# Kernel optimization log

Measured on AMD Instinct MI355X. Metric: run time of the kernel, lower is better.

The kernel has to match this reference:

```python
import jax, jax.numpy as jnp
import numpy as np

N_HEAD = 16
HEAD_DIM = 128  # module's n_embd (per-head)
SEQ = 2048
BATCH = 4
D_MODEL = N_HEAD * HEAD_DIM  # 2048, also input feature dim


def setup_inputs() -> dict:
    key = jax.random.key(0)
    ks = jax.random.split(key, 7)
    scale = 1.0 / np.sqrt(D_MODEL)
    x = jax.random.normal(ks[0], (BATCH, SEQ, D_MODEL), dtype=jnp.float32)
    Wq = jax.random.normal(ks[1], (D_MODEL, D_MODEL), dtype=jnp.float32) * scale
    Wk = jax.random.normal(ks[2], (D_MODEL, D_MODEL), dtype=jnp.float32) * scale
    Wv = jax.random.normal(ks[3], (D_MODEL, D_MODEL), dtype=jnp.float32) * scale
    bq = jnp.zeros((D_MODEL,), dtype=jnp.float32)
    bk = jnp.zeros((D_MODEL,), dtype=jnp.float32)
    bv = jnp.zeros((D_MODEL,), dtype=jnp.float32)
    return {"x": x, "Wq": Wq, "bq": bq, "Wk": Wk, "bk": bk, "Wv": Wv, "bv": bv}


def reference(x, Wq, bq, Wk, bk, Wv, bv):
    B, S, _ = x.shape
    H, D = N_HEAD, HEAD_DIM
    # QKV projections, split heads: [B, H, S, D]
    q = (x @ Wq + bq).reshape(B, S, H, D).transpose(0, 2, 1, 3)
    k = (x @ Wk + bk).reshape(B, S, H, D).transpose(0, 2, 1, 3)
    v = (x @ Wv + bv).reshape(B, S, H, D).transpose(0, 2, 1, 3)
    # scaled dot-product scores [B, H, S, S]
    att = jnp.einsum('bhqd,bhkd->bhqk', q, k) * (1.0 / jnp.sqrt(jnp.float32(D)))
    # causal mask: query i attends to keys j <= i
    causal = jnp.tril(jnp.ones((S, S), dtype=bool))
    att = jnp.where(causal, att, -jnp.inf)
    att = jax.nn.softmax(att, axis=-1)
    # dropout is deterministic (train=False) -> identity
    y = jnp.einsum('bhqk,bhkd->bhqd', att, v)  # [B, H, S, D]
    return y.transpose(0, 2, 1, 3).reshape(B, S, H * D)
```

## Files before the change

### kernel.cpp

```cpp
#include <hip/hip_runtime.h>
#include <hip/hip_bf16.h>
#include <stdint.h>

#define DEVI __device__ __forceinline__

using bf16 = __hip_bfloat16;

typedef __bf16 bf16x8 __attribute__((ext_vector_type(8)));
typedef float f32x4 __attribute__((ext_vector_type(4)));

constexpr int BATCH = 4, NH = 16, SEQ = 2048, HD = 128, DMODEL = 2048;
constexpr int MROWS = BATCH * SEQ;

DEVI f32x4 mfma16(uint4 a, uint4 b, f32x4 c) {
  return __builtin_amdgcn_mfma_f32_16x16x32_bf16(
      __builtin_bit_cast(bf16x8, a), __builtin_bit_cast(bf16x8, b), c, 0, 0, 0);
}

DEVI unsigned pack2(float a, float b) {
  __hip_bfloat16 ha = __float2bfloat16(a), hb = __float2bfloat16(b);
  unsigned short ua = __builtin_bit_cast(unsigned short, ha);
  unsigned short ub = __builtin_bit_cast(unsigned short, hb);
  return ((unsigned)ub << 16) | (unsigned)ua;
}

DEVI void gload16(const void* g, void* l) {
  auto gp = reinterpret_cast<__attribute__((address_space(1))) unsigned int*>(
      reinterpret_cast<uintptr_t>(g));
  auto lp = reinterpret_cast<__attribute__((address_space(3))) unsigned int*>(
      reinterpret_cast<uintptr_t>(l));
  __builtin_amdgcn_global_load_lds(gp, lp, 16, 0, 0);
}

__global__ void cast_x_kernel(const float* __restrict__ in, bf16* __restrict__ out, int n8) {
  for (int i = blockIdx.x * blockDim.x + threadIdx.x; i < n8; i += gridDim.x * blockDim.x) {
    const float4* p = (const float4*)in + (size_t)i * 2;
    float4 a = p[0], b = p[1];
    uint4 u;
    u.x = pack2(a.x, a.y);
    u.y = pack2(a.z, a.w);
    u.z = pack2(b.x, b.y);
    u.w = pack2(b.z, b.w);
    *((uint4*)out + i) = u;
  }
}

__global__ void transpose_w_kernel(const float* __restrict__ W0, const float* __restrict__ W1,
                                   const float* __restrict__ W2, bf16* __restrict__ WtBase) {
  const int z = blockIdx.z;
  const float* W = (z == 0) ? W0 : (z == 1) ? W1 : W2;
  bf16* Wt = WtBase + (size_t)z * DMODEL * DMODEL;
  __shared__ float tile[64][65];
  const int k0 = blockIdx.x * 64, n0 = blockIdx.y * 64;
  const int tid = threadIdx.x;
  for (int i = tid; i < 4096; i += 256) {
    int r = i >> 6, c = i & 63;
    tile[r][c] = W[(size_t)(k0 + r) * DMODEL + n0 + c];
  }
  __syncthreads();
  for (int i = tid; i < 4096; i += 256) {
    int r = i >> 6, c = i & 63;
    Wt[(size_t)(n0 + r) * DMODEL + k0 + c] = __float2bfloat16(tile[c][r]);
  }
}

__global__ __launch_bounds__(256) void gemm_bf16(
    const bf16* __restrict__ A, const bf16* __restrict__ Bt,
    const float* __restrict__ bias, bf16* __restrict__ Cout, int transposed) {
  __shared__ __align__(16) bf16 As[128][32];
  __shared__ __align__(16) bf16 Bs[128][32];
  const int tid = threadIdx.x;
  const int lane = tid & 63, wave = tid >> 6;
  const int lr = lane & 15, lg = lane >> 4;
  const int m0 = blockIdx.x * 128, n0 = blockIdx.y * 128;
  const int wr = wave >> 1, wc = wave & 1;

  f32x4 acc[4][4];
#pragma unroll
  for (int i = 0; i < 4; ++i)
#pragma unroll
    for (int j = 0; j < 4; ++j) acc[i][j] = (f32x4){0.f, 0.f, 0.f, 0.f};

  const char* ag = (const char*)(A + (size_t)(m0 + (tid >> 2)) * DMODEL) + (tid & 3) * 16;
  const char* bg = (const char*)(Bt + (size_t)(n0 + (tid >> 2)) * DMODEL) + (tid & 3) * 16;
  char* asw = (char*)As + wave * 1024;
  char* bsw = (char*)Bs + wave * 1024;
  constexpr size_t rowadv = (size_t)64 * DMODEL * 2;

  for (int k0 = 0; k0 < DMODEL; k0 += 32) {
    gload16(ag + k0 * 2, asw);
    gload16(ag + k0 * 2 + rowadv, asw + 4096);
    gload16(bg + k0 * 2, bsw);
    gload16(bg + k0 * 2 + rowadv, bsw + 4096);
    __syncthreads();
    uint4 af[4], bfr[4];
#pragma unroll
    for (int i = 0; i < 4; ++i) af[i] = *(const uint4*)&As[wr * 64 + i * 16 + lr][lg * 8];
#pragma unroll
    for (int j = 0; j < 4; ++j) bfr[j] = *(const uint4*)&Bs[wc * 64 + j * 16 + lr][lg * 8];
#pragma unroll
    for (int i = 0; i < 4; ++i)
#pragma unroll
      for (int j = 0; j < 4; ++j) acc[i][j] = mfma16(af[i], bfr[j], acc[i][j]);
    __syncthreads();
  }

  float bvals[4];
#pragma unroll
  for (int nf = 0; nf < 4; ++nf) bvals[nf] = bias[n0 + wc * 64 + nf * 16 + lr];

  const int bh = ((m0 >> 11) << 4) | (n0 >> 7);
  const int sbase = (m0 & 2047) + wr * 64;
  if (!transposed) {
    bf16* base = Cout + (size_t)bh * SEQ * HD;
#pragma unroll
    for (int mf = 0; mf < 4; ++mf)
#pragma unroll
      for (int nf = 0; nf < 4; ++nf) {
        int d = wc * 64 + nf * 16 + lr;
#pragma unroll
        for (int jj = 0; jj < 4; ++jj) {
          int s = sbase + mf * 16 + lg * 4 + jj;
          base[(size_t)s * HD + d] = __float2bfloat16(acc[mf][nf][jj] + bvals[nf]);
        }
      }
  } else {
    bf16* base = Cout + (size_t)bh * HD * SEQ;
#pragma unroll
    for (int mf = 0; mf < 4; ++mf)
#pragma unroll
      for (int nf = 0; nf < 4; ++nf) {
        int d = wc * 64 + nf * 16 + lr;
        int s0 = sbase + mf * 16 + lg * 4;
        uint2 u;
        u.x = pack2(acc[mf][nf][0] + bvals[nf], acc[mf][nf][1] + bvals[nf]);
        u.y = pack2(acc[mf][nf][2] + bvals[nf], acc[mf][nf][3] + bvals[nf]);
        *(uint2*)&base[(size_t)d * SEQ + s0] = u;
      }
  }
}

__global__ __launch_bounds__(256) void attn_kernel(
    const bf16* __restrict__ Q, const bf16* __restrict__ K,
    const bf16* __restrict__ Vt, float* __restrict__ out) {
  extern __shared__ __align__(16) char smem[];
  char* KsB = smem;
  char* VsB = smem + 32768;
  char* plB = smem + 65536;

  const int tid = threadIdx.x;
  const int lane = tid & 63;
  const int wave = tid >> 6;
  const int lr = lane & 15, lg = lane >> 4;
  const unsigned swl = ((unsigned)(lr & 7)) << 4;

  const int lid = blockIdx.x;
  const int xcd = lid & 7, slot = lid >> 3;
  const int bh = xcd * 8 + (slot >> 3);
  const int pi = slot & 7;
  const int b = bh >> 4, h = bh & 15;

  const bf16* Qp = Q + (size_t)bh * SEQ * HD;
  const char* Kg0 = (const char*)(K + (size_t)bh * SEQ * HD);
  const char* Vg0 = (const char*)(Vt + (size_t)bh * HD * SEQ);
  char* pbase = plB + wave * 4096;

  const float C2 = 0.08838834764831845f * 1.44269504088896f;
  int cur = 0;

  for (int sec = 0; sec < 2; ++sec) {
    const int qt = (sec == 0) ? pi : (15 - pi);
    const int q0 = qt * 128 + wave * 32;
    const int nt = 2 * qt + 2;
    const int nt_w = (q0 + 95) >> 6;

    uint4 qfrag[2][4];
#pragma unroll
    for (int qf = 0; qf < 2; ++qf) {
      const bf16* qrow = Qp + (size_t)(q0 + qf * 16 + lr) * HD + lg * 8;
#pragma unroll
      for (int dc = 0; dc < 4; ++dc) qfrag[qf][dc] = *(const uint4*)(qrow + dc * 32);
    }

    f32x4 acc[8][2];
#pragma unroll
    for (int df = 0; df < 8; ++df) {
      acc[df][0] = (f32x4){0.f, 0.f, 0.f, 0.f};
      acc[df][1] = (f32x4){0.f, 0.f, 0.f, 0.f};
    }
    float m_run[2] = {-1e30f, -1e30f};
    float l_run[2] = {0.f, 0.f};
    const int qg[2] = {q0 + lr, q0 + 16 + lr};

    {
      const char* Kg = Kg0;
      const char* Vg = Vg0;
      char* kl = KsB + cur * 16384 + wave * 1024;
      char* vl = VsB + cur * 16384 + wave * 1024;
#pragma unroll
      for (int r = 0; r < 4; ++r) {
        int o = r * 4096 + tid * 16;
        int krow = o >> 8; unsigned kcb = o & 255;
        gload16(Kg + krow * 256 + (kcb ^ (((unsigned)(krow & 7)) << 4)), kl + r * 4096);
        int vrow = o >> 7; unsigned vcb = o & 127;
        gload16(Vg + (size_t)vrow * 4096 + (vcb ^ (((unsigned)(vrow & 7)) << 4)), vl + r * 4096);
      }
    }
    __syncthreads();

    for (int t = 0; t < nt; ++t) {
      if (t + 1 < nt) {
        const char* Kg = Kg0 + ((size_t)(t + 1) << 14);
        const char* Vg = Vg0 + ((size_t)(t + 1) << 7);
        char* kl = KsB + (cur ^ 1) * 16384 + wave * 1024;
        char* vl = VsB + (cur ^ 1) * 16384 + wave * 1024;
#pragma unroll
        for (int r = 0; r < 4; ++r) {
          int o = r * 4096 + tid * 16;
          int krow = o >> 8; unsigned kcb = o & 255;
          gload16(Kg + krow * 256 + (kcb ^ (((unsigned)(krow & 7)) << 4)), kl + r * 4096);
          int vrow = o >> 7; unsigned vcb = o & 127;
          gload16(Vg + (size_t)vrow * 4096 + (vcb ^ (((unsigned)(vrow & 7)) << 4)), vl + r * 4096);
        }
      }

      if (t < nt_w) {
        const int kv0 = t << 6;
        const char* kb = KsB + cur * 16384;
        const char* vb = VsB + cur * 16384;

        f32x4 sfr[4][2];
#pragma unroll
        for (int kvf = 0; kvf < 4; ++kvf) {
          sfr[kvf][0] = (f32x4){0.f, 0.f, 0.f, 0.f};
          sfr[kvf][1] = (f32x4){0.f, 0.f, 0.f, 0.f};
          const char* krow = kb + (kvf * 16 + lr) * 256;
#pragma unroll
          for (int dc = 0; dc < 4; ++dc) {
            uint4 ka = *(const uint4*)(krow + (((unsigned)(dc * 64 + lg * 16)) ^ swl));
            sfr[kvf][0] = mfma16(ka, qfrag[0][dc], sfr[kvf][0]);
            sfr[kvf][1] = mfma16(ka, qfrag[1][dc], sfr[kvf][1]);
          }
        }

        const bool need_mask = (kv0 + 63) > q0;
#pragma unroll
        for (int qf = 0; qf < 2; ++qf) {
          float mx = -1e30f;
#pragma unroll
          for (int kvf = 0; kvf < 4; ++kvf)
#pragma unroll
            for (int j = 0; j < 4; ++j) {
              float v = sfr[kvf][qf][j] * C2;
              if (need_mask) {
                int kvgl = kv0 + kvf * 16 + lg * 4 + j;
                v = (kvgl <= qg[qf]) ? v : -1e30f;
              }
              sfr[kvf][qf][j] = v;
              mx = fmaxf(mx, v);
            }
          mx = fmaxf(mx, __shfl_xor(mx, 16));
          mx = fmaxf(mx, __shfl_xor(mx, 32));
          float mnew = fmaxf(m_run[qf], mx);
          float corr = exp2f(m_run[qf] - mnew);
          m_run[qf] = mnew;
          float ps = 0.f;
          const int qlocal = qf * 16 + lr;
          const unsigned sw = ((unsigned)(qlocal & 7)) << 4;
          char* bp = pbase + qlocal * 128;
#pragma unroll
          for (int kvf = 0; kvf < 4; ++kvf) {
            float p0 = exp2f(sfr[kvf][qf][0] - mnew);
            float p1 = exp2f(sfr[kvf][qf][1] - mnew);
            float p2 = exp2f(sfr[kvf][qf][2] - mnew);
            float p3 = exp2f(sfr[kvf][qf][3] - mnew);
            ps += p0 + p1 + p2 + p3;
            unsigned off = ((unsigned)(kvf * 32 + lg * 8)) ^ sw;
            *(unsigned*)(bp + off) = pack2(p0, p1);
            *(unsigned*)(bp + off + 4) = pack2(p2, p3);
          }
          ps += __shfl_xor(ps, 16);
          ps += __shfl_xor(ps, 32);
          l_run[qf] = l_run[qf] * corr + ps;
#pragma unroll
          for (int df = 0; df < 8; ++df) acc[df][qf] *= corr;
        }
        asm volatile("s_waitcnt lgkmcnt(0)" ::: "memory");

        uint4 pb[2][2];
#pragma unroll
        for (int qf = 0; qf < 2; ++qf) {
          const int qlocal = qf * 16 + lr;
          const unsigned sw = ((unsigned)(qlocal & 7)) << 4;
          char* bp = pbase + qlocal * 128;
          pb[0][qf] = *(uint4*)(bp + (((unsigned)(lg * 16)) ^ sw));
          pb[1][qf] = *(uint4*)(bp + (((unsigned)(64 + lg * 16)) ^ sw));
        }

#pragma unroll
        for (int df = 0; df < 8; ++df) {
          const char* vrow = vb + (df * 16 + lr) * 128;
          uint4 va0 = *(const uint4*)(vrow + (((unsigned)(lg * 16)) ^ swl));
          uint4 va1 = *(const uint4*)(vrow + (((unsigned)(64 + lg * 16)) ^ swl));
          acc[df][0] = mfma16(va0, pb[0][0], acc[df][0]);
          acc[df][1] = mfma16(va0, pb[0][1], acc[df][1]);
          acc[df][0] = mfma16(va1, pb[1][0], acc[df][0]);
          acc[df][1] = mfma16(va1, pb[1][1], acc[df][1]);
        }
      }

      __syncthreads();
      cur ^= 1;
    }

#pragma unroll
    for (int qf = 0; qf < 2; ++qf) {
      float inv = 1.f / l_run[qf];
      size_t rowoff = ((size_t)b * SEQ + (size_t)(q0 + qf * 16 + lr)) * DMODEL + h * HD;
#pragma unroll
      for (int df = 0; df < 8; ++df) {
        float4 o;
        o.x = acc[df][qf][0] * inv;
        o.y = acc[df][qf][1] * inv;
        o.z = acc[df][qf][2] * inv;
        o.w = acc[df][qf][3] * inv;
        *(float4*)(out + rowoff + df * 16 + lg * 4) = o;
      }
    }
  }
}

extern "C" void kernel_launch(void* const* d_in, const int* in_sizes, int n_in,
                              void* d_out, int out_size, void* d_ws, size_t ws_size,
                              hipStream_t stream) {
  const float* x = (const float*)d_in[0];
  const float* Wq = (const float*)d_in[1];
  const float* bq = (const float*)d_in[2];
  const float* Wk = (const float*)d_in[3];
  const float* bk = (const float*)d_in[4];
  const float* Wv = (const float*)d_in[5];
  const float* bv = (const float*)d_in[6];
  float* out = (float*)d_out;

  const size_t sz_x = (size_t)MROWS * DMODEL * 2;
  const size_t sz_w = (size_t)DMODEL * DMODEL * 2;
  const size_t sz_qkv = (size_t)MROWS * DMODEL * 2;
  if (ws_size < sz_x + 3 * sz_w + 3 * sz_qkv) return;

  char* w = (char*)d_ws;
  bf16* xb = (bf16*)w;  w += sz_x;
  bf16* WtQ = (bf16*)w; w += sz_w;
  bf16* WtK = (bf16*)w; w += sz_w;
  bf16* WtV = (bf16*)w; w += sz_w;
  bf16* Qb = (bf16*)w;  w += sz_qkv;
  bf16* Kb = (bf16*)w;  w += sz_qkv;
  bf16* Vtb = (bf16*)w; w += sz_qkv;

  cast_x_kernel<<<2048, 256, 0, stream>>>(x, xb, MROWS * DMODEL / 8);
  transpose_w_kernel<<<dim3(32, 32, 3), 256, 0, stream>>>(Wq, Wk, Wv, WtQ);
  gemm_bf16<<<dim3(64, 16), 256, 0, stream>>>(xb, WtQ, bq, Qb, 0);
  gemm_bf16<<<dim3(64, 16), 256, 0, stream>>>(xb, WtK, bk, Kb, 0);
  gemm_bf16<<<dim3(64, 16), 256, 0, stream>>>(xb, WtV, bv, Vtb, 1);
  attn_kernel<<<dim3(512), 256, 81920, stream>>>(Qb, Kb, Vtb, out);
}
```

Before: 636.5 us.

## Double-buffer GEMM tiles and restructure attention with 512 threads, direct V loads

The projection GEMM gets double-buffered shared-memory tiles so the next K-slice loads while MFMAs run on the current one, and one barrier per iteration is dropped. The attention kernel moves to 8 waves of 16 query rows each, stops staging V in LDS and reads V fragments straight from global memory, and shrinks LDS use so more blocks can fit per CU. It also adds a lazy softmax rescale that skips correcting the accumulator unless the row max grows past a threshold. The direct V reads rely on cache hits instead of LDS reuse, and the lazy rescale risks larger intermediate exponent values.

```diff
diff --git a/kernel.cpp b/kernel.cpp
--- a/kernel.cpp
+++ b/kernel.cpp
@@ -67,8 +67,8 @@
 __global__ __launch_bounds__(256) void gemm_bf16(
     const bf16* __restrict__ A, const bf16* __restrict__ Bt,
     const float* __restrict__ bias, bf16* __restrict__ Cout, int transposed) {
-  __shared__ __align__(16) bf16 As[128][32];
-  __shared__ __align__(16) bf16 Bs[128][32];
+  __shared__ __align__(16) bf16 As[2][128][32];
+  __shared__ __align__(16) bf16 Bs[2][128][32];
   const int tid = threadIdx.x;
   const int lane = tid & 63, wave = tid >> 6;
   const int lr = lane & 15, lg = lane >> 4;
@@ -87,22 +87,32 @@
   char* bsw = (char*)Bs + wave * 1024;
   constexpr size_t rowadv = (size_t)64 * DMODEL * 2;
 
+  gload16(ag, asw);
+  gload16(ag + rowadv, asw + 4096);
+  gload16(bg, bsw);
+  gload16(bg + rowadv, bsw + 4096);
+  __syncthreads();
+
+  int cur = 0;
   for (int k0 = 0; k0 < DMODEL; k0 += 32) {
-    gload16(ag + k0 * 2, asw);
-    gload16(ag + k0 * 2 + rowadv, asw + 4096);
-    gload16(bg + k0 * 2, bsw);
-    gload16(bg + k0 * 2 + rowadv, bsw + 4096);
-    __syncthreads();
+    if (k0 + 32 < DMODEL) {
+      int nb = (cur ^ 1) * 8192;
+      gload16(ag + (k0 + 32) * 2, asw + nb);
+      gload16(ag + (k0 + 32) * 2 + rowadv, asw + nb + 4096);
+      gload16(bg + (k0 + 32) * 2, bsw + nb);
+      gload16(bg + (k0 + 32) * 2 + rowadv, bsw + nb + 4096);
+    }
     uint4 af[4], bfr[4];
 #pragma unroll
-    for (int i = 0; i < 4; ++i) af[i] = *(const uint4*)&As[wr * 64 + i * 16 + lr][lg * 8];
-#pragma unroll
-    for (int j = 0; j < 4; ++j) bfr[j] = *(const uint4*)&Bs[wc * 64 + j * 16 + lr][lg * 8];
+    for (int i = 0; i < 4; ++i) af[i] = *(const uint4*)&As[cur][wr * 64 + i * 16 + lr][lg * 8];
+#pragma unroll
+    for (int j = 0; j < 4; ++j) bfr[j] = *(const uint4*)&Bs[cur][wc * 64 + j * 16 + lr][lg * 8];
 #pragma unroll
     for (int i = 0; i < 4; ++i)
 #pragma unroll
       for (int j = 0; j < 4; ++j) acc[i][j] = mfma16(af[i], bfr[j], acc[i][j]);
     __syncthreads();
+    cur ^= 1;
   }
 
   float bvals[4];
@@ -140,13 +150,12 @@
   }
 }
 
-__global__ __launch_bounds__(256) void attn_kernel(
+__global__ __launch_bounds__(512, 4) void attn_kernel(
     const bf16* __restrict__ Q, const bf16* __restrict__ K,
     const bf16* __restrict__ Vt, float* __restrict__ out) {
   extern __shared__ __align__(16) char smem[];
   char* KsB = smem;
-  char* VsB = smem + 32768;
-  char* plB = smem + 65536;
+  char* plB = smem + 32768;
 
   const int tid = threadIdx.x;
   const int lane = tid & 63;
@@ -162,48 +171,39 @@
 
   const bf16* Qp = Q + (size_t)bh * SEQ * HD;
   const char* Kg0 = (const char*)(K + (size_t)bh * SEQ * HD);
-  const char* Vg0 = (const char*)(Vt + (size_t)bh * HD * SEQ);
-  char* pbase = plB + wave * 4096;
+  const bf16* Vp = Vt + (size_t)bh * HD * SEQ;
+  char* bp = plB + wave * 2304 + lr * 144;
 
   const float C2 = 0.08838834764831845f * 1.44269504088896f;
+  const float THR = 8.0f;
   int cur = 0;
 
   for (int sec = 0; sec < 2; ++sec) {
     const int qt = (sec == 0) ? pi : (15 - pi);
-    const int q0 = qt * 128 + wave * 32;
+    const int q0 = qt * 128 + wave * 16;
     const int nt = 2 * qt + 2;
-    const int nt_w = (q0 + 95) >> 6;
-
-    uint4 qfrag[2][4];
-#pragma unroll
-    for (int qf = 0; qf < 2; ++qf) {
-      const bf16* qrow = Qp + (size_t)(q0 + qf * 16 + lr) * HD + lg * 8;
-#pragma unroll
-      for (int dc = 0; dc < 4; ++dc) qfrag[qf][dc] = *(const uint4*)(qrow + dc * 32);
-    }
-
-    f32x4 acc[8][2];
-#pragma unroll
-    for (int df = 0; df < 8; ++df) {
-      acc[df][0] = (f32x4){0.f, 0.f, 0.f, 0.f};
-      acc[df][1] = (f32x4){0.f, 0.f, 0.f, 0.f};
-    }
-    float m_run[2] = {-1e30f, -1e30f};
-    float l_run[2] = {0.f, 0.f};
-    const int qg[2] = {q0 + lr, q0 + 16 + lr};
-
+    const int nt_w = (q0 + 79) >> 6;
+    const int qg = q0 + lr;
+
+    uint4 qfrag[4];
     {
-      const char* Kg = Kg0;
-      const char* Vg = Vg0;
-      char* kl = KsB + cur * 16384 + wave * 1024;
-      char* vl = VsB + cur * 16384 + wave * 1024;
-#pragma unroll
-      for (int r = 0; r < 4; ++r) {
-        int o = r * 4096 + tid * 16;
+      const bf16* qrow = Qp + (size_t)qg * HD + lg * 8;
+#pragma unroll
+      for (int dc = 0; dc < 4; ++dc) qfrag[dc] = *(const uint4*)(qrow + dc * 32);
+    }
+
+    f32x4 acc[8];
+#pragma unroll
+    for (int df = 0; df < 8; ++df) acc[df] = (f32x4){0.f, 0.f, 0.f, 0.f};
+    float m_run = -1e30f, l_run = 0.f;
+
+    {
+      char* kl = KsB + cur * 16384 + tid * 16;
+#pragma unroll
+      for (int r = 0; r < 2; ++r) {
+        int o = r * 8192 + tid * 16;
         int krow = o >> 8; unsigned kcb = o & 255;
-        gload16(Kg + krow * 256 + (kcb ^ (((unsigned)(krow & 7)) << 4)), kl + r * 4096);
-        int vrow = o >> 7; unsigned vcb = o & 127;
-        gload16(Vg + (size_t)vrow * 4096 + (vcb ^ (((unsigned)(vrow & 7)) << 4)), vl + r * 4096);
+        gload16(Kg0 + krow * 256 + (kcb ^ (((unsigned)(krow & 7)) << 4)), kl + r * 8192);
       }
     }
     __syncthreads();
@@ -211,101 +211,83 @@
     for (int t = 0; t < nt; ++t) {
       if (t + 1 < nt) {
         const char* Kg = Kg0 + ((size_t)(t + 1) << 14);
-        const char* Vg = Vg0 + ((size_t)(t + 1) << 7);
-        char* kl = KsB + (cur ^ 1) * 16384 + wave * 1024;
-        char* vl = VsB + (cur ^ 1) * 16384 + wave * 1024;
-#pragma unroll
-        for (int r = 0; r < 4; ++r) {
-          int o = r * 4096 + tid * 16;
+        char* kl = KsB + (cur ^ 1) * 16384 + tid * 16;
+#pragma unroll
+        for (int r = 0; r < 2; ++r) {
+          int o = r * 8192 + tid * 16;
           int krow = o >> 8; unsigned kcb = o & 255;
-          gload16(Kg + krow * 256 + (kcb ^ (((unsigned)(krow & 7)) << 4)), kl + r * 4096);
-          int vrow = o >> 7; unsigned vcb = o & 127;
-          gload16(Vg + (size_t)vrow * 4096 + (vcb ^ (((unsigned)(vrow & 7)) << 4)), vl + r * 4096);
+          gload16(Kg + krow * 256 + (kcb ^ (((unsigned)(krow & 7)) << 4)), kl + r * 8192);
         }
       }
 
       if (t < nt_w) {
         const int kv0 = t << 6;
         const char* kb = KsB + cur * 16384;
-        const char* vb = VsB + cur * 16384;
-
-        f32x4 sfr[4][2];
+
+        f32x4 sfr[4];
 #pragma unroll
         for (int kvf = 0; kvf < 4; ++kvf) {
-          sfr[kvf][0] = (f32x4){0.f, 0.f, 0.f, 0.f};
-          sfr[kvf][1] = (f32x4){0.f, 0.f, 0.f, 0.f};
+          sfr[kvf] = (f32x4){0.f, 0.f, 0.f, 0.f};
           const char* krow = kb + (kvf * 16 + lr) * 256;
 #pragma unroll
           for (int dc = 0; dc < 4; ++dc) {
             uint4 ka = *(const uint4*)(krow + (((unsigned)(dc * 64 + lg * 16)) ^ swl));
-            sfr[kvf][0] = mfma16(ka, qfrag[0][dc], sfr[kvf][0]);
-            sfr[kvf][1] = mfma16(ka, qfrag[1][dc], sfr[kvf][1]);
+            sfr[kvf] = mfma16(ka, qfrag[dc], sfr[kvf]);
           }
         }
 
         const bool need_mask = (kv0 + 63) > q0;
-#pragma unroll
-        for (int qf = 0; qf < 2; ++qf) {
-          float mx = -1e30f;
-#pragma unroll
-          for (int kvf = 0; kvf < 4; ++kvf)
-#pragma unroll
-            for (int j = 0; j < 4; ++j) {
-              float v = sfr[kvf][qf][j] * C2;
-              if (need_mask) {
-                int kvgl = kv0 + kvf * 16 + lg * 4 + j;
-                v = (kvgl <= qg[qf]) ? v : -1e30f;
-              }
-              sfr[kvf][qf][j] = v;
-              mx = fmaxf(mx, v);
+        float mx = -1e30f;
+#pragma unroll
+        for (int kvf = 0; kvf < 4; ++kvf)
+#pragma unroll
+          for (int j = 0; j < 4; ++j) {
+            float v = sfr[kvf][j] * C2;
+            if (need_mask) {
+              int kvgl = kv0 + kvf * 16 + lg * 4 + j;
+              v = (kvgl <= qg) ? v : -1e30f;
             }
-          mx = fmaxf(mx, __shfl_xor(mx, 16));
-          mx = fmaxf(mx, __shfl_xor(mx, 32));
-          float mnew = fmaxf(m_run[qf], mx);
-          float corr = exp2f(m_run[qf] - mnew);
-          m_run[qf] = mnew;
-          float ps = 0.f;
-          const int qlocal = qf * 16 + lr;
-          const unsigned sw = ((unsigned)(qlocal & 7)) << 4;
-          char* bp = pbase + qlocal * 128;
-#pragma unroll
-          for (int kvf = 0; kvf < 4; ++kvf) {
-            float p0 = exp2f(sfr[kvf][qf][0] - mnew);
-            float p1 = exp2f(sfr[kvf][qf][1] - mnew);
-            float p2 = exp2f(sfr[kvf][qf][2] - mnew);
-            float p3 = exp2f(sfr[kvf][qf][3] - mnew);
-            ps += p0 + p1 + p2 + p3;
-            unsigned off = ((unsigned)(kvf * 32 + lg * 8)) ^ sw;
-            *(unsigned*)(bp + off) = pack2(p0, p1);
-            *(unsigned*)(bp + off + 4) = pack2(p2, p3);
+            sfr[kvf][j] = v;
+            mx = fmaxf(mx, v);
           }
-          ps += __shfl_xor(ps, 16);
-          ps += __shfl_xor(ps, 32);
-          l_run[qf] = l_run[qf] * corr + ps;
-#pragma unroll
-          for (int df = 0; df < 8; ++df) acc[df][qf] *= corr;
-        }
+        mx = fmaxf(mx, __shfl_xor(mx, 16));
+        mx = fmaxf(mx, __shfl_xor(mx, 32));
+        if (!__all(mx <= m_run + THR)) {
+          float mnew = fmaxf(m_run, mx);
+          float corr = exp2f(m_run - mnew);
+          l_run *= corr;
+#pragma unroll
+          for (int df = 0; df < 8; ++df) acc[df] *= corr;
+          m_run = mnew;
+        }
+        float ps = 0.f;
+#pragma unroll
+        for (int kvf = 0; kvf < 4; ++kvf) {
+          float p0 = exp2f(sfr[kvf][0] - m_run);
+          float p1 = exp2f(sfr[kvf][1] - m_run);
+          float p2 = exp2f(sfr[kvf][2] - m_run);
+          float p3 = exp2f(sfr[kvf][3] - m_run);
+          ps += p0 + p1 + p2 + p3;
+          unsigned off = (unsigned)(kvf * 32 + lg * 8);
+          *(unsigned*)(bp + off) = pack2(p0, p1);
+          *(unsigned*)(bp + off + 4) = pack2(p2, p3);
+        }
+        ps += __shfl_xor(ps, 16);
+        ps += __shfl_xor(ps, 32);
+        l_run += ps;
+
         asm volatile("s_waitcnt lgkmcnt(0)" ::: "memory");
 
-        uint4 pb[2][2];
-#pragma unroll
-        for (int qf = 0; qf < 2; ++qf) {
-          const int qlocal = qf * 16 + lr;
-          const unsigned sw = ((unsigned)(qlocal & 7)) << 4;
-          char* bp = pbase + qlocal * 128;
-          pb[0][qf] = *(uint4*)(bp + (((unsigned)(lg * 16)) ^ sw));
-          pb[1][qf] = *(uint4*)(bp + (((unsigned)(64 + lg * 16)) ^ sw));
-        }
+        uint4 pb0 = *(uint4*)(bp + lg * 16);
+        uint4 pb1 = *(uint4*)(bp + 64 + lg * 16);
 
 #pragma unroll
         for (int df = 0; df < 8; ++df) {
-          const char* vrow = vb + (df * 16 + lr) * 128;
-          uint4 va0 = *(const uint4*)(vrow + (((unsigned)(lg * 16)) ^ swl));
-          uint4 va1 = *(const uint4*)(vrow + (((unsigned)(64 + lg * 16)) ^ swl));
-          acc[df][0] = mfma16(va0, pb[0][0], acc[df][0]);
-          acc[df][1] = mfma16(va0, pb[0][1], acc[df][1]);
-          acc[df][0] = mfma16(va1, pb[1][0], acc[df][0]);
-          acc[df][1] = mfma16(va1, pb[1][1], acc[df][1]);
+          const bf16* vrow = Vp + (size_t)(df * 16 + lr) * SEQ + kv0 + lg * 8;
+          uint4 va0 = *(const uint4*)(vrow);
+          uint4 va1 = *(const uint4*)(vrow + 32);
+          acc[df] = mfma16(va0, pb0, acc[df]);
+          acc[df] = mfma16(va1, pb1, acc[df]);
         }
       }
 
@@ -313,17 +295,16 @@
       cur ^= 1;
     }
 
-#pragma unroll
-    for (int qf = 0; qf < 2; ++qf) {
-      float inv = 1.f / l_run[qf];
-      size_t rowoff = ((size_t)b * SEQ + (size_t)(q0 + qf * 16 + lr)) * DMODEL + h * HD;
+    {
+      float inv = 1.f / l_run;
+      size_t rowoff = ((size_t)b * SEQ + (size_t)qg) * DMODEL + h * HD;
 #pragma unroll
       for (int df = 0; df < 8; ++df) {
         float4 o;
-        o.x = acc[df][qf][0] * inv;
-        o.y = acc[df][qf][1] * inv;
-        o.z = acc[df][qf][2] * inv;
-        o.w = acc[df][qf][3] * inv;
+        o.x = acc[df][0] * inv;
+        o.y = acc[df][1] * inv;
+        o.z = acc[df][2] * inv;
+        o.w = acc[df][3] * inv;
         *(float4*)(out + rowoff + df * 16 + lg * 4) = o;
       }
     }
@@ -361,5 +342,5 @@
   gemm_bf16<<<dim3(64, 16), 256, 0, stream>>>(xb, WtQ, bq, Qb, 0);
   gemm_bf16<<<dim3(64, 16), 256, 0, stream>>>(xb, WtK, bk, Kb, 0);
   gemm_bf16<<<dim3(64, 16), 256, 0, stream>>>(xb, WtV, bv, Vtb, 1);
-  attn_kernel<<<dim3(512), 256, 81920, stream>>>(Qb, Kb, Vtb, out);
-}
+  attn_kernel<<<dim3(512), 512, 51200, stream>>>(Qb, Kb, Vtb, out);
+}
```

New measurement: 708.2 us. 1.11x slower.

## Double-buffer GEMM, keep P in registers, lazy softmax rescale in attention

Applied to the files above, without the earlier changes.

The GEMM gets double-buffered LDS tiles so the next K-slice loads overlap the MFMAs, an XCD-aware block remap, and a swapped operand order for Q/K so the epilogue writes packed, vectorized rows. Attention drops the LDS round trip for P by feeding register fragments straight into 16x16x16 bf16 MFMAs, and rescales the running max only when it grows past a threshold. It also shrinks shared memory and sets launch bounds to allow two blocks per CU. The trade-offs are twice as many PV MFMA instructions, higher register pressure, and the numeric assumption that exp2 stays bounded when the max is not updated.

```diff
diff --git a/kernel.cpp b/kernel.cpp
--- a/kernel.cpp
+++ b/kernel.cpp
@@ -7,14 +7,27 @@
 using bf16 = __hip_bfloat16;
 
 typedef __bf16 bf16x8 __attribute__((ext_vector_type(8)));
+typedef short s16x4 __attribute__((ext_vector_type(4)));
 typedef float f32x4 __attribute__((ext_vector_type(4)));
 
 constexpr int BATCH = 4, NH = 16, SEQ = 2048, HD = 128, DMODEL = 2048;
 constexpr int MROWS = BATCH * SEQ;
 
-DEVI f32x4 mfma16(uint4 a, uint4 b, f32x4 c) {
+DEVI f32x4 mfma32(uint4 a, uint4 b, f32x4 c) {
   return __builtin_amdgcn_mfma_f32_16x16x32_bf16(
       __builtin_bit_cast(bf16x8, a), __builtin_bit_cast(bf16x8, b), c, 0, 0, 0);
+}
+
+DEVI f32x4 mfma16k(uint2 a, uint2 b, f32x4 c) {
+#if __has_builtin(__builtin_amdgcn_mfma_f32_16x16x16bf16_1k)
+  return __builtin_amdgcn_mfma_f32_16x16x16bf16_1k(
+      __builtin_bit_cast(s16x4, a), __builtin_bit_cast(s16x4, b), c, 0, 0, 0);
+#else
+  f32x4 d;
+  asm("v_mfma_f32_16x16x16_bf16 %0, %1, %2, %3"
+      : "=v"(d) : "v"(a), "v"(b), "v"(c));
+  return d;
+#endif
 }
 
 DEVI unsigned pack2(float a, float b) {
@@ -64,15 +77,19 @@
   }
 }
 
+template <int TR>
 __global__ __launch_bounds__(256) void gemm_bf16(
     const bf16* __restrict__ A, const bf16* __restrict__ Bt,
-    const float* __restrict__ bias, bf16* __restrict__ Cout, int transposed) {
-  __shared__ __align__(16) bf16 As[128][32];
-  __shared__ __align__(16) bf16 Bs[128][32];
+    const float* __restrict__ bias, bf16* __restrict__ Cout) {
+  __shared__ __align__(16) bf16 As[2][128][32];
+  __shared__ __align__(16) bf16 Bs[2][128][32];
   const int tid = threadIdx.x;
   const int lane = tid & 63, wave = tid >> 6;
   const int lr = lane & 15, lg = lane >> 4;
-  const int m0 = blockIdx.x * 128, n0 = blockIdx.y * 128;
+  const int lid = blockIdx.y * gridDim.x + blockIdx.x;
+  const int g = lid & 7, kk = lid >> 3;
+  const int m0 = (kk & 63) * 128;
+  const int n0 = ((g << 1) | (kk >> 6)) * 128;
   const int wr = wave >> 1, wc = wave & 1;
 
   f32x4 acc[4][4];
@@ -87,44 +104,60 @@
   char* bsw = (char*)Bs + wave * 1024;
   constexpr size_t rowadv = (size_t)64 * DMODEL * 2;
 
+  gload16(ag, asw);
+  gload16(ag + rowadv, asw + 4096);
+  gload16(bg, bsw);
+  gload16(bg + rowadv, bsw + 4096);
+  __syncthreads();
+
+  int cur = 0;
   for (int k0 = 0; k0 < DMODEL; k0 += 32) {
-    gload16(ag + k0 * 2, asw);
-    gload16(ag + k0 * 2 + rowadv, asw + 4096);
-    gload16(bg + k0 * 2, bsw);
-    gload16(bg + k0 * 2 + rowadv, bsw + 4096);
+    if (k0 + 32 < DMODEL) {
+      int nb = (cur ^ 1) * 8192;
+      gload16(ag + (k0 + 32) * 2, asw + nb);
+      gload16(ag + (k0 + 32) * 2 + rowadv, asw + nb + 4096);
+      gload16(bg + (k0 + 32) * 2, bsw + nb);
+      gload16(bg + (k0 + 32) * 2 + rowadv, bsw + nb + 4096);
+    }
+    uint4 af[4], bfr[4];
+#pragma unroll
+    for (int i = 0; i < 4; ++i) af[i] = *(const uint4*)&As[cur][wr * 64 + i * 16 + lr][lg * 8];
+#pragma unroll
+    for (int j = 0; j < 4; ++j) bfr[j] = *(const uint4*)&Bs[cur][wc * 64 + j * 16 + lr][lg * 8];
+#pragma unroll
+    for (int i = 0; i < 4; ++i)
+#pragma unroll
+      for (int j = 0; j < 4; ++j) {
+        if (TR == 0)
+          acc[i][j] = mfma32(bfr[j], af[i], acc[i][j]);
+        else
+          acc[i][j] = mfma32(af[i], bfr[j], acc[i][j]);
+      }
     __syncthreads();
-    uint4 af[4], bfr[4];
-#pragma unroll
-    for (int i = 0; i < 4; ++i) af[i] = *(const uint4*)&As[wr * 64 + i * 16 + lr][lg * 8];
-#pragma unroll
-    for (int j = 0; j < 4; ++j) bfr[j] = *(const uint4*)&Bs[wc * 64 + j * 16 + lr][lg * 8];
-#pragma unroll
-    for (int i = 0; i < 4; ++i)
-#pragma unroll
-      for (int j = 0; j < 4; ++j) acc[i][j] = mfma16(af[i], bfr[j], acc[i][j]);
-    __syncthreads();
-  }
-
-  float bvals[4];
-#pragma unroll
-  for (int nf = 0; nf < 4; ++nf) bvals[nf] = bias[n0 + wc * 64 + nf * 16 + lr];
+    cur ^= 1;
+  }
 
   const int bh = ((m0 >> 11) << 4) | (n0 >> 7);
   const int sbase = (m0 & 2047) + wr * 64;
-  if (!transposed) {
+  if (TR == 0) {
     bf16* base = Cout + (size_t)bh * SEQ * HD;
 #pragma unroll
-    for (int mf = 0; mf < 4; ++mf)
-#pragma unroll
-      for (int nf = 0; nf < 4; ++nf) {
-        int d = wc * 64 + nf * 16 + lr;
-#pragma unroll
-        for (int jj = 0; jj < 4; ++jj) {
-          int s = sbase + mf * 16 + lg * 4 + jj;
-          base[(size_t)s * HD + d] = __float2bfloat16(acc[mf][nf][jj] + bvals[nf]);
-        }
-      }
+    for (int j = 0; j < 4; ++j) {
+      const int d0 = wc * 64 + j * 16 + lg * 4;
+      float4 bb = *(const float4*)&bias[n0 + d0];
+#pragma unroll
+      for (int i = 0; i < 4; ++i) {
+        int s = sbase + i * 16 + lr;
+        uint2 u;
+        u.x = pack2(acc[i][j][0] + bb.x, acc[i][j][1] + bb.y);
+        u.y = pack2(acc[i][j][2] + bb.z, acc[i][j][3] + bb.w);
+        *(uint2*)&base[(size_t)s * HD + d0] = u;
+      }
+    }
   } else {
+    float bvals[4];
+#pragma unroll
+    for (int nf = 0; nf < 4; ++nf) bvals[nf] = bias[n0 + wc * 64 + nf * 16 + lr];
     bf16* base = Cout + (size_t)bh * HD * SEQ;
 #pragma unroll
     for (int mf = 0; mf < 4; ++mf)
@@ -140,13 +173,12 @@
   }
 }
 
-__global__ __launch_bounds__(256) void attn_kernel(
+__global__ __launch_bounds__(256, 2) void attn_kernel(
     const bf16* __restrict__ Q, const bf16* __restrict__ K,
     const bf16* __restrict__ Vt, float* __restrict__ out) {
   extern __shared__ __align__(16) char smem[];
   char* KsB = smem;
   char* VsB = smem + 32768;
-  char* plB = smem + 65536;
 
   const int tid = threadIdx.x;
   const int lane = tid & 63;
@@ -163,9 +195,9 @@
   const bf16* Qp = Q + (size_t)bh * SEQ * HD;
   const char* Kg0 = (const char*)(K + (size_t)bh * SEQ * HD);
   const char* Vg0 = (const char*)(Vt + (size_t)bh * HD * SEQ);
-  char* pbase = plB + wave * 4096;
 
   const float C2 = 0.08838834764831845f * 1.44269504088896f;
+  const float THR = 8.0f;
   int cur = 0;
 
   for (int sec = 0; sec < 2; ++sec) {
@@ -173,6 +205,7 @@
     const int q0 = qt * 128 + wave * 32;
     const int nt = 2 * qt + 2;
     const int nt_w = (q0 + 95) >> 6;
+    const int qg[2] = {q0 + lr, q0 + 16 + lr};
 
     uint4 qfrag[2][4];
 #pragma unroll
@@ -190,20 +223,17 @@
     }
     float m_run[2] = {-1e30f, -1e30f};
     float l_run[2] = {0.f, 0.f};
-    const int qg[2] = {q0 + lr, q0 + 16 + lr};
 
     {
-      const char* Kg = Kg0;
-      const char* Vg = Vg0;
-      char* kl = KsB + cur * 16384 + wave * 1024;
-      char* vl = VsB + cur * 16384 + wave * 1024;
+      char* kl = KsB + cur * 16384 + tid * 16;
+      char* vl = VsB + cur * 16384 + tid * 16;
 #pragma unroll
       for (int r = 0; r < 4; ++r) {
         int o = r * 4096 + tid * 16;
         int krow = o >> 8; unsigned kcb = o & 255;
-        gload16(Kg + krow * 256 + (kcb ^ (((unsigned)(krow & 7)) << 4)), kl + r * 4096);
+        gload16(Kg0 + krow * 256 + (kcb ^ (((unsigned)(krow & 7)) << 4)), kl + r * 4096);
         int vrow = o >> 7; unsigned vcb = o & 127;
-        gload16(Vg + (size_t)vrow * 4096 + (vcb ^ (((unsigned)(vrow & 7)) << 4)), vl + r * 4096);
+        gload16(Vg0 + (size_t)vrow * 4096 + (vcb ^ (((unsigned)(vrow & 7)) << 4)), vl + r * 4096);
       }
     }
     __syncthreads();
@@ -212,8 +242,8 @@
       if (t + 1 < nt) {
         const char* Kg = Kg0 + ((size_t)(t + 1) << 14);
         const char* Vg = Vg0 + ((size_t)(t + 1) << 7);
-        char* kl = KsB + (cur ^ 1) * 16384 + wave * 1024;
-        char* vl = VsB + (cur ^ 1) * 16384 + wave * 1024;
+        char* kl = KsB + (cur ^ 1) * 16384 + tid * 16;
+        char* vl = VsB + (cur ^ 1) * 16384 + tid * 16;
 #pragma unroll
         for (int r = 0; r < 4; ++r) {
           int o = r * 4096 + tid * 16;
@@ -238,11 +268,12 @@
 #pragma unroll
           for (int dc = 0; dc < 4; ++dc) {
             uint4 ka = *(const uint4*)(krow + (((unsigned)(dc * 64 + lg * 16)) ^ swl));
-            sfr[kvf][0] = mfma16(ka, qfrag[0][dc], sfr[kvf][0]);
-            sfr[kvf][1] = mfma16(ka, qfrag[1][dc], sfr[kvf][1]);
+            sfr[kvf][0] = mfma32(ka, qfrag[0][dc], sfr[kvf][0]);
+            sfr[kvf][1] = mfma32(ka, qfrag[1][dc], sfr[kvf][1]);
           }
         }
 
+        uint2 pfrag[4][2];
         const bool need_mask = (kv0 + 63) > q0;
 #pragma unroll
         for (int qf = 0; qf < 2; ++qf) {
@@ -261,51 +292,39 @@
             }
           mx = fmaxf(mx, __shfl_xor(mx, 16));
           mx = fmaxf(mx, __shfl_xor(mx, 32));
-          float mnew = fmaxf(m_run[qf], mx);
-          float corr = exp2f(m_run[qf] - mnew);
-          m_run[qf] = mnew;
+          if (!__all(mx <= m_run[qf] + THR)) {
+            float mnew = fmaxf(m_run[qf], mx);
+            float corr = exp2f(m_run[qf] - mnew);
+            l_run[qf] *= corr;
+#pragma unroll
+            for (int df = 0; df < 8; ++df) acc[df][qf] *= corr;
+            m_run[qf] = mnew;
+          }
           float ps = 0.f;
-          const int qlocal = qf * 16 + lr;
-          const unsigned sw = ((unsigned)(qlocal & 7)) << 4;
-          char* bp = pbase + qlocal * 128;
 #pragma unroll
           for (int kvf = 0; kvf < 4; ++kvf) {
-            float p0 = exp2f(sfr[kvf][qf][0] - mnew);
-            float p1 = exp2f(sfr[kvf][qf][1] - mnew);
-            float p2 = exp2f(sfr[kvf][qf][2] - mnew);
-            float p3 = exp2f(sfr[kvf][qf][3] - mnew);
+            float p0 = exp2f(sfr[kvf][qf][0] - m_run[qf]);
+            float p1 = exp2f(sfr[kvf][qf][1] - m_run[qf]);
+            float p2 = exp2f(sfr[kvf][qf][2] - m_run[qf]);
+            float p3 = exp2f(sfr[kvf][qf][3] - m_run[qf]);
             ps += p0 + p1 + p2 + p3;
-            unsigned off = ((unsigned)(kvf * 32 + lg * 8)) ^ sw;
-            *(unsigned*)(bp + off) = pack2(p0, p1);
-            *(unsigned*)(bp + off + 4) = pack2(p2, p3);
+            pfrag[kvf][qf].x = pack2(p0, p1);
+            pfrag[kvf][qf].y = pack2(p2, p3);
           }
           ps += __shfl_xor(ps, 16);
           ps += __shfl_xor(ps, 32);
-          l_run[qf] = l_run[qf] * corr + ps;
-#pragma unroll
-          for (int df = 0; df < 8; ++df) acc[df][qf] *= corr;
-        }
-        asm volatile("s_waitcnt lgkmcnt(0)" ::: "memory");
-
-        uint4 pb[2][2];
-#pragma unroll
-        for (int qf = 0; qf < 2; ++qf) {
-          const int qlocal = qf * 16 + lr;
-          const unsigned sw = ((unsigned)(qlocal & 7)) << 4;
-          char* bp = pbase + qlocal * 128;
-          pb[0][qf] = *(uint4*)(bp + (((unsigned)(lg * 16)) ^ sw));
-          pb[1][qf] = *(uint4*)(bp + (((unsigned)(64 + lg * 16)) ^ sw));
+          l_run[qf] += ps;
         }
 
 #pragma unroll
         for (int df = 0; df < 8; ++df) {
           const char* vrow = vb + (df * 16 + lr) * 128;
-          uint4 va0 = *(const uint4*)(vrow + (((unsigned)(lg * 16)) ^ swl));
-          uint4 va1 = *(const uint4*)(vrow + (((unsigned)(64 + lg * 16)) ^ swl));
-          acc[df][0] = mfma16(va0, pb[0][0], acc[df][0]);
-          acc[df][1] = mfma16(va0, pb[0][1], acc[df][1]);
-          acc[df][0] = mfma16(va1, pb[1][0], acc[df][0]);
-          acc[df][1] = mfma16(va1, pb[1][1], acc[df][1]);
+#pragma unroll
+          for (int kvf = 0; kvf < 4; ++kvf) {
+            uint2 va = *(const uint2*)(vrow + (((unsigned)(kvf * 32 + lg * 8)) ^ swl));
+            acc[df][0] = mfma16k(va, pfrag[kvf][0], acc[df][0]);
+            acc[df][1] = mfma16k(va, pfrag[kvf][1], acc[df][1]);
+          }
         }
       }
 
@@ -316,7 +335,7 @@
 #pragma unroll
     for (int qf = 0; qf < 2; ++qf) {
       float inv = 1.f / l_run[qf];
-      size_t rowoff = ((size_t)b * SEQ + (size_t)(q0 + qf * 16 + lr)) * DMODEL + h * HD;
+      size_t rowoff = ((size_t)b * SEQ + (size_t)qg[qf]) * DMODEL + h * HD;
 #pragma unroll
       for (int df = 0; df < 8; ++df) {
         float4 o;
@@ -358,8 +377,8 @@
 
   cast_x_kernel<<<2048, 256, 0, stream>>>(x, xb, MROWS * DMODEL / 8);
   transpose_w_kernel<<<dim3(32, 32, 3), 256, 0, stream>>>(Wq, Wk, Wv, WtQ);
-  gemm_bf16<<<dim3(64, 16), 256, 0, stream>>>(xb, WtQ, bq, Qb, 0);
-  gemm_bf16<<<dim3(64, 16), 256, 0, stream>>>(xb, WtK, bk, Kb, 0);
-  gemm_bf16<<<dim3(64, 16), 256, 0, stream>>>(xb, WtV, bv, Vtb, 1);
-  attn_kernel<<<dim3(512), 256, 81920, stream>>>(Qb, Kb, Vtb, out);
-}
+  gemm_bf16<0><<<dim3(64, 16), 256, 0, stream>>>(xb, WtQ, bq, Qb);
+  gemm_bf16<0><<<dim3(64, 16), 256, 0, stream>>>(xb, WtK, bk, Kb);
+  gemm_bf16<1><<<dim3(64, 16), 256, 0, stream>>>(xb, WtV, bv, Vtb);
+  attn_kernel<<<dim3(512), 256, 65536, stream>>>(Qb, Kb, Vtb, out);
+}
```

After: 586.8 us. -7.8%, faster.
